# Kernel optimization log

Measured on AMD Instinct MI355X. Metric: run time of the kernel, lower is better.

## Reference

```python
import jax, jax.numpy as jnp
import numpy as np

EPS = 1e-5

def _lin_bn_relu(x, W, b, gamma, beta):
    # x: [N, Cin], W: [Cout, Cin] (torch layout), b/gamma/beta: [Cout]
    y = x @ W.T + b
    mu = jnp.mean(y, axis=0)                      # training-mode batch stats
    var = jnp.mean((y - mu) ** 2, axis=0)         # biased variance (torch BN)
    yhat = (y - mu) * jax.lax.rsqrt(var + EPS)
    return jax.nn.relu(gamma * yhat + beta)


def setup_inputs() -> dict:
    key = jax.random.key(0)
    ks = jax.random.split(key, 16)
    N = 262144
    dims = [(64, 3), (512, 64), (512, 512), (2, 512)]
    inp = {
        "x1": jax.random.normal(ks[0], (8, 4, 8, 8), dtype=jnp.float32),
        "x2": jax.random.normal(ks[1], (N, 3), dtype=jnp.float32),
    }
    for i, (co, ci) in enumerate(dims, start=1):
        lim = 1.0 / np.sqrt(ci)
        inp[f"W{i}"] = jax.random.uniform(ks[2 * i], (co, ci), jnp.float32, -lim, lim)
        inp[f"b{i}"] = jax.random.uniform(ks[2 * i + 1], (co,), jnp.float32, -lim, lim)
    for i, c in enumerate([64, 512, 512], start=1):
        inp[f"gamma{i}"] = jnp.ones((c,), jnp.float32)
        inp[f"beta{i}"] = jnp.zeros((c,), jnp.float32)
    return inp


def reference(x1, x2, W1, b1, W2, b2, W3, b3, W4, b4,
              gamma1, beta1, gamma2, beta2, gamma3, beta3):
    # x1 is sliced in the original forward (x[0][:, 0:-1]) but unused in the output.
    h = _lin_bn_relu(x2, W1, b1, gamma1, beta1)   # [N, 64]
    h = _lin_bn_relu(h, W2, b2, gamma2, beta2)    # [N, 512]
    h = _lin_bn_relu(h, W3, b3, gamma3, beta3)    # [N, 512]
    out = h @ W4.T + b4                           # [N, 2]
    return out
```

## Files before the change

kernel.cpp:

```cpp
#include <hip/hip_runtime.h>

typedef __bf16 bf16x4 __attribute__((ext_vector_type(4)));
typedef __bf16 bf16x8 __attribute__((ext_vector_type(8)));
typedef float f32x4 __attribute__((ext_vector_type(4)));

#define MFMA_BF16 __builtin_amdgcn_mfma_f32_16x16x32_bf16

__global__ __launch_bounds__(256) void prep_xmom_kernel(
    const float* __restrict__ x, const float* __restrict__ W2,
    const float* __restrict__ W3, __bf16* __restrict__ W2bf,
    __bf16* __restrict__ W3bf, float* __restrict__ xmom) {
  const int b = blockIdx.x;
  const int t = threadIdx.x;
  if (b >= 64) {
    const float* src;
    __bf16* dst;
    int idx;
    if (b < 80) {
      idx = (b - 64) * 2048 + t * 8;
      src = W2;
      dst = W2bf;
    } else {
      idx = (b - 80) * 2048 + t * 8;
      src = W3;
      dst = W3bf;
    }
    float4 f0 = *(const float4*)(src + idx);
    float4 f1 = *(const float4*)(src + idx + 4);
    bf16x8 o;
    o[0] = (__bf16)f0.x;
    o[1] = (__bf16)f0.y;
    o[2] = (__bf16)f0.z;
    o[3] = (__bf16)f0.w;
    o[4] = (__bf16)f1.x;
    o[5] = (__bf16)f1.y;
    o[6] = (__bf16)f1.z;
    o[7] = (__bf16)f1.w;
    *(bf16x8*)(dst + idx) = o;
    return;
  }
  float m[9] = {};
#pragma unroll 4
  for (int i = 0; i < 16; ++i) {
    int r = b * 4096 + i * 256 + t;
    const float* xp = x + (size_t)r * 3;
    float a = xp[0], bb = xp[1], c = xp[2];
    m[0] += a;
    m[1] += bb;
    m[2] += c;
    m[3] = fmaf(a, a, m[3]);
    m[4] = fmaf(a, bb, m[4]);
    m[5] = fmaf(a, c, m[5]);
    m[6] = fmaf(bb, bb, m[6]);
    m[7] = fmaf(bb, c, m[7]);
    m[8] = fmaf(c, c, m[8]);
  }
  __shared__ float red[4][9];
  int lane = t & 63, wave = t >> 6;
#pragma unroll
  for (int j = 0; j < 9; ++j) {
    float v = m[j];
    v += __shfl_xor(v, 1);
    v += __shfl_xor(v, 2);
    v += __shfl_xor(v, 4);
    v += __shfl_xor(v, 8);
    v += __shfl_xor(v, 16);
    v += __shfl_xor(v, 32);
    if (lane == 0) red[wave][j] = v;
  }
  __syncthreads();
  if (t < 9) atomicAdd(&xmom[t], red[0][t] + red[1][t] + red[2][t] + red[3][t]);
}

__device__ __forceinline__ void bn1_fold(const float* __restrict__ xm,
                                         const float* __restrict__ W1,
                                         const float* __restrict__ b1,
                                         const float* __restrict__ gamma1,
                                         const float* __restrict__ beta1,
                                         int c, float invN, float fN,
                                         float* f0, float* f1, float* f2,
                                         float* f3) {
  float w0 = W1[c * 3], w1 = W1[c * 3 + 1], w2 = W1[c * 3 + 2], bb = b1[c];
  float wx = w0 * xm[0] + w1 * xm[1] + w2 * xm[2];
  float sy = wx + fN * bb;
  float q = w0 * w0 * xm[3] + 2.f * w0 * w1 * xm[4] + 2.f * w0 * w2 * xm[5] +
            w1 * w1 * xm[6] + 2.f * w1 * w2 * xm[7] + w2 * w2 * xm[8] +
            2.f * bb * wx + fN * bb * bb;
  float mu = sy * invN;
  float var = q * invN - mu * mu;
  float sc = gamma1[c] * rsqrtf(var + 1e-5f);
  float sh = beta1[c] - mu * sc;
  *f0 = sc * w0;
  *f1 = sc * w1;
  *f2 = sc * w2;
  *f3 = sc * bb + sh;
}

__global__ __launch_bounds__(256, 4) void m1_kernel(
    const float* __restrict__ x2, const float* __restrict__ xmom,
    const float* __restrict__ gamma1, const float* __restrict__ beta1,
    const float* __restrict__ W1, const float* __restrict__ b1,
    float* __restrict__ M1, float* __restrict__ s1, float invN, float fN) {
  __shared__ float sF[256];
  __shared__ float xs[768];
  __shared__ __bf16 h1T[64 * 264];
  __shared__ float s1s[4][64];

  const int t = threadIdx.x;
  const int lane = t & 63, wave = t >> 6;
  const int lrow = lane & 15, lgrp = lane >> 4;

  if (t < 64) {
    float f0, f1, f2, f3;
    bn1_fold(xmom, W1, b1, gamma1, beta1, t, invN, fN, &f0, &f1, &f2, &f3);
    sF[t] = f0;
    sF[64 + t] = f1;
    sF[128 + t] = f2;
    sF[192 + t] = f3;
  }
  if (t < 192)
    ((float4*)xs)[t] = ((const float4*)(x2 + (size_t)blockIdx.x * 768))[t];
  __syncthreads();

  const int c0 = (t & 3) * 16;
  const int r0 = t >> 2;
  float sAcc[16] = {};
#pragma unroll
  for (int s = 0; s < 4; ++s) {
    int r = r0 + s * 64;
    float X0 = xs[r * 3], X1 = xs[r * 3 + 1], X2 = xs[r * 3 + 2];
#pragma unroll
    for (int j = 0; j < 16; ++j) {
      int c = c0 + j;
      float h = fmaxf(
          fmaf(sF[c], X0, fmaf(sF[64 + c], X1, fmaf(sF[128 + c], X2, sF[192 + c]))),
          0.f);
      sAcc[j] += h;
      h1T[c * 264 + r] = (__bf16)h;
    }
  }
  __syncthreads();

  f32x4 acc[4] = {};
#pragma unroll
  for (int kk = 0; kk < 256; kk += 32) {
    bf16x8 af = *(const bf16x8*)&h1T[(wave * 16 + lrow) * 264 + kk + lgrp * 8];
#pragma unroll
    for (int n = 0; n < 4; ++n) {
      bf16x8 bfr = *(const bf16x8*)&h1T[(n * 16 + lrow) * 264 + kk + lgrp * 8];
      acc[n] = MFMA_BF16(af, bfr, acc[n], 0, 0, 0);
    }
  }
#pragma unroll
  for (int n = 0; n < 4; ++n)
#pragma unroll
    for (int rr = 0; rr < 4; ++rr)
      atomicAdd(&M1[(wave * 16 + lgrp * 4 + rr) * 64 + n * 16 + lrow],
                acc[n][rr]);

#pragma unroll
  for (int j = 0; j < 16; ++j) {
    float v = sAcc[j];
    v += __shfl_xor(v, 4);
    v += __shfl_xor(v, 8);
    v += __shfl_xor(v, 16);
    v += __shfl_xor(v, 32);
    if (lane < 4) s1s[wave][(lane & 3) * 16 + j] = v;
  }
  __syncthreads();
  if (t < 64)
    atomicAdd(&s1[t], s1s[0][t] + s1s[1][t] + s1s[2][t] + s1s[3][t]);
}

__global__ __launch_bounds__(256) void finalize2v_kernel(
    const float* __restrict__ M1, const float* __restrict__ s1,
    const float* __restrict__ W2, const float* __restrict__ b2,
    const float* __restrict__ gamma2, const float* __restrict__ beta2,
    float* __restrict__ scale2, float* __restrict__ shift2f, float fN) {
  __shared__ float sM[64 * 65];
  __shared__ float ss[64];
  int t = threadIdx.x;
  for (int i = t; i < 4096; i += 256) sM[(i >> 6) * 65 + (i & 63)] = M1[i];
  if (t < 64) ss[t] = s1[t];
  __syncthreads();
  int lane = t & 63;
  int col = blockIdx.x * 4 + (t >> 6);
  float wi = W2[(size_t)col * 64 + lane];
  float p = 0.f;
#pragma unroll
  for (int j = 0; j < 64; ++j) p = fmaf(sM[lane * 65 + j], __shfl(wi, j), p);
  float qi = wi * p;
  float swi = ss[lane] * wi;
#pragma unroll
  for (int off = 1; off < 64; off <<= 1) {
    qi += __shfl_xor(qi, off);
    swi += __shfl_xor(swi, off);
  }
  if (lane == 0) {
    float b = b2[col];
    float sy = swi + fN * b;
    float sqs = qi + 2.f * b * swi + fN * b * b;
    float mu = sy / fN;
    float var = sqs / fN - mu * mu;
    float sc = gamma2[col] * rsqrtf(var + 1e-5f);
    scale2[col] = sc;
    shift2f[col] = (beta2[col] - mu * sc) + sc * b;
  }
}

#define G3_LD(BUF, K)                                                        \
  _Pragma("unroll") for (int m = 0; m < 4; ++m) BUF[m] =                     \
      *(const bf16x8*)&h2r[(m * 16 + lrow) * 520 + (K) * 32 + lgrp * 8];

#define G3_MM(BUF, K)                                                        \
  _Pragma("unroll") for (int m = 0; m < 4; ++m) {                            \
    acc[m][0] = MFMA_BF16(BUF[m], b3r[K][0], acc[m][0], 0, 0, 0);            \
    acc[m][1] = MFMA_BF16(BUF[m], b3r[K][1], acc[m][1], 0, 0, 0);            \
  }

template <int MODE>
__global__ __launch_bounds__(512, 2) void fused_kernel(
    const float* __restrict__ x2, const float* __restrict__ xmom,
    const float* __restrict__ gamma1, const float* __restrict__ beta1,
    const float* __restrict__ W1, const float* __restrict__ b1,
    const __bf16* __restrict__ W2bf, const float* __restrict__ scale2,
    const float* __restrict__ shift2f, const __bf16* __restrict__ W3bf,
    const float* __restrict__ b3, const float* __restrict__ gamma3,
    const float* __restrict__ beta3, const float* __restrict__ W4,
    const float* __restrict__ b4, float* __restrict__ gsum3,
    float* __restrict__ gsq3, float* __restrict__ out,
    __bf16* __restrict__ y3o, int gBase, int gCount, int rStoreRgs,
    float invN, float fN) {
  __shared__ __bf16 h1buf[2][64 * 72];
  __shared__ __bf16 h2buf[2][64 * 520];
  __shared__ float sF[256];
  __shared__ float sSc2[512], sSh2[512];
  __shared__ float outaccW[8][64][2];

  const int t = threadIdx.x;
  const int lane = t & 63, wave = t >> 6;
  const int lrow = lane & 15, lgrp = lane >> 4;
  const int colHalf = blockIdx.x & 1;
  const int rgFirst = gBase + (int)(blockIdx.x >> 1) * gCount;
  const int wCol3 = colHalf * 256 + wave * 32;
  const int wCol2 = wave * 64;

  if (t < 64) {
    float f0, f1, f2, f3;
    bn1_fold(xmom, W1, b1, gamma1, beta1, t, invN, fN, &f0, &f1, &f2, &f3);
    sF[t] = f0;
    sF[64 + t] = f1;
    sF[128 + t] = f2;
    sF[192 + t] = f3;
  }
  sSc2[t] = scale2[t & 511];
  sSh2[t] = shift2f[t & 511];

  bf16x8 b2r[2][4];
#pragma unroll
  for (int kk = 0; kk < 2; ++kk)
#pragma unroll
    for (int n = 0; n < 4; ++n)
      b2r[kk][n] = *(const bf16x8*)&W2bf[(wCol2 + n * 16 + lrow) * 64 +
                                         kk * 32 + lgrp * 8];
  bf16x8 b3r[16][2];
#pragma unroll
  for (int k = 0; k < 16; ++k)
#pragma unroll
    for (int n = 0; n < 2; ++n)
      b3r[k][n] = *(const bf16x8*)&W3bf[(size_t)(wCol3 + n * 16 + lrow) * 512 +
                                        k * 32 + lgrp * 8];

  const int c3a = wCol3 + lrow, c3b = wCol3 + 16 + lrow;
  float b3a = 0.f, b3b = 0.f;
  float sc3a = 0.f, sc3b = 0.f, sh3a = 0.f, sh3b = 0.f;
  float w40a = 0.f, w40b = 0.f, w41a = 0.f, w41b = 0.f, B40 = 0.f, B41 = 0.f;
  if (MODE != 2) {
    b3a = b3[c3a];
    b3b = b3[c3b];
  } else {
    float mu = gsum3[c3a] * invN;
    float var = gsq3[c3a] * invN - mu * mu;
    sc3a = gamma3[c3a] * rsqrtf(var + 1e-5f);
    sh3a = sc3a * b3[c3a] + (beta3[c3a] - mu * sc3a);
    mu = gsum3[c3b] * invN;
    var = gsq3[c3b] * invN - mu * mu;
    sc3b = gamma3[c3b] * rsqrtf(var + 1e-5f);
    sh3b = sc3b * b3[c3b] + (beta3[c3b] - mu * sc3b);
    w40a = W4[c3a];
    w40b = W4[c3b];
    w41a = W4[512 + c3a];
    w41b = W4[512 + c3b];
    B40 = b4[0];
    B41 = b4[1];
  }
  float csA = 0.f, cqA = 0.f, csB = 0.f, cqB = 0.f;

  const int hr = t >> 3, hc0 = (t & 7) * 8;
  const float* xbase = x2 + ((size_t)rgFirst * 64 + hr) * 3;
  float xa, xb, xc;

  auto stageH1 = [&](__bf16* h1p) {
    bf16x8 hv;
#pragma unroll
    for (int j = 0; j < 8; ++j) {
      int c = hc0 + j;
      float h = fmaf(sF[c], xa,
                     fmaf(sF[64 + c], xb, fmaf(sF[128 + c], xc, sF[192 + c])));
      hv[j] = (__bf16)fmaxf(h, 0.f);
    }
    *(bf16x8*)&h1p[hr * 72 + hc0] = hv;
  };

  auto gemm2 = [&](const __bf16* h1p, __bf16* h2p) {
#pragma unroll
    for (int nh = 0; nh < 2; ++nh) {
      f32x4 a2[2][4] = {};
#pragma unroll
      for (int kk = 0; kk < 2; ++kk) {
        bf16x8 af0 = *(const bf16x8*)&h1p[(0 * 16 + lrow) * 72 + kk * 32 + lgrp * 8];
        bf16x8 af1 = *(const bf16x8*)&h1p[(1 * 16 + lrow) * 72 + kk * 32 + lgrp * 8];
        bf16x8 af2 = *(const bf16x8*)&h1p[(2 * 16 + lrow) * 72 + kk * 32 + lgrp * 8];
        bf16x8 af3 = *(const bf16x8*)&h1p[(3 * 16 + lrow) * 72 + kk * 32 + lgrp * 8];
#pragma unroll
        for (int n2 = 0; n2 < 2; ++n2) {
          int n = nh * 2 + n2;
          a2[n2][0] = MFMA_BF16(b2r[kk][n], af0, a2[n2][0], 0, 0, 0);
          a2[n2][1] = MFMA_BF16(b2r[kk][n], af1, a2[n2][1], 0, 0, 0);
          a2[n2][2] = MFMA_BF16(b2r[kk][n], af2, a2[n2][2], 0, 0, 0);
          a2[n2][3] = MFMA_BF16(b2r[kk][n], af3, a2[n2][3], 0, 0, 0);
        }
      }
#pragma unroll
      for (int n2 = 0; n2 < 2; ++n2) {
        int ch0 = wCol2 + (nh * 2 + n2) * 16 + lgrp * 4;
        float s0 = sSc2[ch0], s1v = sSc2[ch0 + 1], s2v = sSc2[ch0 + 2],
              s3v = sSc2[ch0 + 3];
        float z0 = sSh2[ch0], z1 = sSh2[ch0 + 1], z2 = sSh2[ch0 + 2],
              z3 = sSh2[ch0 + 3];
#pragma unroll
        for (int m = 0; m < 4; ++m) {
          int row = m * 16 + lrow;
          bf16x4 hv;
          hv[0] = (__bf16)fmaxf(fmaf(s0, a2[n2][m][0], z0), 0.f);
          hv[1] = (__bf16)fmaxf(fmaf(s1v, a2[n2][m][1], z1), 0.f);
          hv[2] = (__bf16)fmaxf(fmaf(s2v, a2[n2][m][2], z2), 0.f);
          hv[3] = (__bf16)fmaxf(fmaf(s3v, a2[n2][m][3], z3), 0.f);
          *(bf16x4*)&h2p[row * 520 + ch0] = hv;
        }
      }
    }
  };

  __syncthreads();

  xa = xbase[0];
  xb = xbase[1];
  xc = xbase[2];
  stageH1(h1buf[0]);
  __syncthreads();
  gemm2(h1buf[0], h2buf[0]);
  if (gCount > 1) {
    const float* xn = xbase + 192;
    xa = xn[0];
    xb = xn[1];
    xc = xn[2];
    stageH1(h1buf[1]);
  }
  __syncthreads();

  for (int g = 0; g < gCount; ++g) {
    const int rBase = (rgFirst + g) * 64;
    const __bf16* h2r = h2buf[g & 1];
    const bool doStore = (MODE == 3) && (rgFirst + g < rStoreRgs);

    if (g + 2 < gCount) {
      const float* xn = xbase + (size_t)(g + 2) * 192;
      xa = xn[0];
      xb = xn[1];
      xc = xn[2];
    }

    if (g + 1 < gCount) gemm2(h1buf[(g + 1) & 1], h2buf[(g + 1) & 1]);

    if (g + 2 < gCount) stageH1(h1buf[g & 1]);

    f32x4 acc[4][2] = {};
    bf16x8 afA[4], afB[4];
    G3_LD(afA, 0)
#pragma unroll
    for (int k = 0; k < 16; k += 2) {
      G3_LD(afB, k + 1)
      G3_MM(afA, k)
      if (k < 14) { G3_LD(afA, k + 2) }
      G3_MM(afB, k + 1)
    }

    if (MODE != 2) {
#pragma unroll
      for (int m = 0; m < 4; ++m)
#pragma unroll
        for (int rr = 0; rr < 4; ++rr) {
          float ya = acc[m][0][rr] + b3a;
          float yb = acc[m][1][rr] + b3b;
          csA += ya;
          cqA = fmaf(ya, ya, cqA);
          csB += yb;
          cqB = fmaf(yb, yb, cqB);
          if (doStore) {
            size_t row = (size_t)(rBase + m * 16 + lgrp * 4 + rr);
            y3o[row * 512 + c3a] = (__bf16)ya;
            y3o[row * 512 + c3b] = (__bf16)yb;
          }
        }
    } else {
#pragma unroll
      for (int m = 0; m < 4; ++m)
#pragma unroll
        for (int rr = 0; rr < 4; ++rr) {
          float ha = fmaxf(fmaf(sc3a, acc[m][0][rr], sh3a), 0.f);
          float hb = fmaxf(fmaf(sc3b, acc[m][1][rr], sh3b), 0.f);
          float dd0 = fmaf(ha, w40a, hb * w40b);
          float dd1 = fmaf(ha, w41a, hb * w41b);
          dd0 += __shfl_xor(dd0, 1);
          dd1 += __shfl_xor(dd1, 1);
          dd0 += __shfl_xor(dd0, 2);
          dd1 += __shfl_xor(dd1, 2);
          dd0 += __shfl_xor(dd0, 4);
          dd1 += __shfl_xor(dd1, 4);
          dd0 += __shfl_xor(dd0, 8);
          dd1 += __shfl_xor(dd1, 8);
          if (lrow == 0) {
            int row = m * 16 + lgrp * 4 + rr;
            outaccW[wave][row][0] = dd0;
            outaccW[wave][row][1] = dd1;
          }
        }
    }
    __syncthreads();
  }

  if (MODE != 2) {
    csA += __shfl_xor(csA, 16);
    cqA += __shfl_xor(cqA, 16);
    csB += __shfl_xor(csB, 16);
    cqB += __shfl_xor(cqB, 16);
    csA += __shfl_xor(csA, 32);
    cqA += __shfl_xor(cqA, 32);
    csB += __shfl_xor(csB, 32);
    cqB += __shfl_xor(cqB, 32);
    if (lgrp == 0) {
      atomicAdd(&gsum3[c3a], csA);
      atomicAdd(&gsq3[c3a], cqA);
      atomicAdd(&gsum3[c3b], csB);
      atomicAdd(&gsq3[c3b], cqB);
    }
  } else {
    if (t < 128) {
      int row = t >> 1, o = t & 1;
      float s = 0.f;
#pragma unroll
      for (int w = 0; w < 8; ++w) s += outaccW[w][row][o];
      if (colHalf == 0) s += (o == 0) ? B40 : B41;
      atomicAdd(&out[(size_t)(rgFirst * 64 + row) * 2 + o], s);
    }
  }
}

__global__ __launch_bounds__(256) void stream_out_kernel(
    const __bf16* __restrict__ y3, const float* __restrict__ gsum3,
    const float* __restrict__ gsq3, const float* __restrict__ gamma3,
    const float* __restrict__ beta3, const float* __restrict__ W4,
    const float* __restrict__ b4, float* __restrict__ out, int N, float invN) {
  __shared__ float sSc[512], sSh[512], sW0[512], sW1[512];
  int t = threadIdx.x;
  for (int i = t; i < 512; i += 256) {
    float mu = gsum3[i] * invN;
    float var = gsq3[i] * invN - mu * mu;
    float sc = gamma3[i] * rsqrtf(var + 1e-5f);
    sSc[i] = sc;
    sSh[i] = beta3[i] - mu * sc;
    sW0[i] = W4[i];
    sW1[i] = W4[512 + i];
  }
  __syncthreads();
  int lane = t & 63, wv = t >> 6;
  int c0 = lane * 8;
  float fsc[8], fsh[8], fw0[8], fw1[8];
#pragma unroll
  for (int j = 0; j < 8; ++j) {
    fsc[j] = sSc[c0 + j];
    fsh[j] = sSh[c0 + j];
    fw0[j] = sW0[c0 + j];
    fw1[j] = sW1[c0 + j];
  }
  float B0 = b4[0], B1 = b4[1];
  for (size_t row = (size_t)blockIdx.x * 8 + wv * 2; row < (size_t)N;
       row += (size_t)gridDim.x * 8) {
    bf16x8 v0 = *(const bf16x8*)(y3 + row * 512 + c0);
    bf16x8 v1 = *(const bf16x8*)(y3 + (row + 1) * 512 + c0);
    float d0a = 0.f, d1a = 0.f, d0b = 0.f, d1b = 0.f;
#pragma unroll
    for (int j = 0; j < 8; ++j) {
      float ha = fmaxf(fmaf(fsc[j], (float)v0[j], fsh[j]), 0.f);
      float hb = fmaxf(fmaf(fsc[j], (float)v1[j], fsh[j]), 0.f);
      d0a = fmaf(ha, fw0[j], d0a);
      d1a = fmaf(ha, fw1[j], d1a);
      d0b = fmaf(hb, fw0[j], d0b);
      d1b = fmaf(hb, fw1[j], d1b);
    }
    float t0 = d0a + __shfl_xor(d0a, 1);
    float t1 = d1a + __shfl_xor(d1a, 1);
    float t2 = d0b + __shfl_xor(d0b, 1);
    float t3 = d1b + __shfl_xor(d1b, 1);
    float u0 = (lane & 1) ? t1 : t0;
    float u1 = (lane & 1) ? t3 : t2;
    u0 += __shfl_xor(u0, 2);
    u1 += __shfl_xor(u1, 2);
    float w = (lane & 2) ? u1 : u0;
    w += __shfl_xor(w, 4);
    w += __shfl_xor(w, 8);
    w += __shfl_xor(w, 16);
    w += __shfl_xor(w, 32);
    if (lane < 4) out[row * 2 + lane] = w + ((lane & 1) ? B1 : B0);
  }
}

extern "C" void kernel_launch(void* const* d_in, const int* in_sizes, int n_in,
                              void* d_out, int out_size, void* d_ws,
                              size_t ws_size, hipStream_t stream) {
  const float* x2 = (const float*)d_in[1];
  const float* W1 = (const float*)d_in[2];
  const float* b1 = (const float*)d_in[3];
  const float* W2 = (const float*)d_in[4];
  const float* b2 = (const float*)d_in[5];
  const float* W3 = (const float*)d_in[6];
  const float* b3 = (const float*)d_in[7];
  const float* W4 = (const float*)d_in[8];
  const float* b4 = (const float*)d_in[9];
  const float* gamma1 = (const float*)d_in[10];
  const float* beta1 = (const float*)d_in[11];
  const float* gamma2 = (const float*)d_in[12];
  const float* beta2 = (const float*)d_in[13];
  const float* gamma3 = (const float*)d_in[14];
  const float* beta3 = (const float*)d_in[15];
  float* out = (float*)d_out;

  const int N = in_sizes[1] / 3;
  const float invN = 1.0f / (float)N;
  const float fN = (float)N;

  float* f0 = (float*)d_ws;
  float* xmom = f0;
  float* M1 = f0 + 16;
  float* s1 = f0 + 4112;
  float* gsum3 = f0 + 4176;
  float* gsq3 = f0 + 4688;
  float* scale2 = f0 + 5200;
  float* shift2f = f0 + 5712;
  __bf16* W2bf = (__bf16*)(f0 + 6224);
  __bf16* W3bf = W2bf + 32768;

  const size_t y3off = (size_t)1 << 20;
  size_t availRows = (ws_size > y3off) ? (ws_size - y3off) / 1024 : 0;
  int rStoreBlks = (int)((availRows / 1024 < (size_t)(N / 1024))
                             ? availRows / 1024
                             : (size_t)(N / 1024));
  const int rStore = rStoreBlks * 1024;
  __bf16* y3bf = (__bf16*)((char*)d_ws + y3off);

  hipMemsetAsync(f0, 0, 5200 * sizeof(float), stream);
  prep_xmom_kernel<<<208, 256, 0, stream>>>(x2, W2, W3, W2bf, W3bf, xmom);
  m1_kernel<<<N / 256, 256, 0, stream>>>(x2, xmom, gamma1, beta1, W1, b1, M1,
                                         s1, invN, fN);
  finalize2v_kernel<<<128, 256, 0, stream>>>(M1, s1, W2, b2, gamma2, beta2,
                                             scale2, shift2f, fN);

  fused_kernel<3><<<(N / 2048) * 2, 512, 0, stream>>>(
      x2, xmom, gamma1, beta1, W1, b1, W2bf, scale2, shift2f, W3bf, b3,
      gamma3, beta3, W4, b4, gsum3, gsq3, out, y3bf, 0, 32, rStoreBlks * 16,
      invN, fN);

  if (rStore > 0)
    stream_out_kernel<<<2048, 256, 0, stream>>>(y3bf, gsum3, gsq3, gamma3,
                                                beta3, W4, b4, out, rStore,
                                                invN);
  if (rStore < N) {
    hipMemsetAsync(out + (size_t)rStore * 2, 0,
                   (size_t)(N - rStore) * 2 * sizeof(float), stream);
    fused_kernel<2><<<((N - rStore) / 64) * 2, 512, 0, stream>>>(
        x2, xmom, gamma1, beta1, W1, b1, W2bf, scale2, shift2f, W3bf, b3,
        gamma3, beta3, W4, b4, gsum3, gsq3, out, y3bf, rStore / 64, 1, 0,
        invN, fN);
  }
}
```

Before: 324.4 us.

## Merge column-half blocks into 1024-thread blocks covering all 512 layer-3 columns

The fused kernel now launches 1024-thread blocks in which 16 waves each own 32 of the 512 layer-3 columns. Previously two 512-thread blocks each recomputed layer 2 for the same row groups and split the columns between them. This removes the duplicated layer-2 GEMM and the duplicated h1 staging. In the fallback mode it also drops the atomic output accumulation and the memset of the output. In exchange each block holds one resident block per CU (launch_bounds 1024,1), there are fewer row groups per block (16 instead of 32), and block-wide syncs now cover 16 waves.

```diff
diff --git a/kernel.cpp b/kernel.cpp
--- a/kernel.cpp
+++ b/kernel.cpp
@@ -219,7 +219,7 @@
   }
 
 template <int MODE>
-__global__ __launch_bounds__(512, 2) void fused_kernel(
+__global__ __launch_bounds__(1024, 1) void fused_kernel(
     const float* __restrict__ x2, const float* __restrict__ xmom,
     const float* __restrict__ gamma1, const float* __restrict__ beta1,
     const float* __restrict__ W1, const float* __restrict__ b1,
@@ -231,19 +231,18 @@
     float* __restrict__ gsq3, float* __restrict__ out,
     __bf16* __restrict__ y3o, int gBase, int gCount, int rStoreRgs,
     float invN, float fN) {
-  __shared__ __bf16 h1buf[2][64 * 72];
-  __shared__ __bf16 h2buf[2][64 * 520];
+  constexpr int NB = (MODE == 2) ? 1 : 2;
+  __shared__ __bf16 h1buf[NB][64 * 72];
+  __shared__ __bf16 h2buf[NB][64 * 520];
   __shared__ float sF[256];
   __shared__ float sSc2[512], sSh2[512];
-  __shared__ float outaccW[8][64][2];
+  __shared__ float outaccW[(MODE == 2) ? 16 : 1][64][2];
 
   const int t = threadIdx.x;
   const int lane = t & 63, wave = t >> 6;
   const int lrow = lane & 15, lgrp = lane >> 4;
-  const int colHalf = blockIdx.x & 1;
-  const int rgFirst = gBase + (int)(blockIdx.x >> 1) * gCount;
-  const int wCol3 = colHalf * 256 + wave * 32;
-  const int wCol2 = wave * 64;
+  const int rgFirst = gBase + (int)blockIdx.x * gCount;
+  const int wCol = wave * 32;
 
   if (t < 64) {
     float f0, f1, f2, f3;
@@ -253,25 +252,27 @@
     sF[128 + t] = f2;
     sF[192 + t] = f3;
   }
-  sSc2[t] = scale2[t & 511];
-  sSh2[t] = shift2f[t & 511];
-
-  bf16x8 b2r[2][4];
+  if (t < 512) {
+    sSc2[t] = scale2[t];
+    sSh2[t] = shift2f[t];
+  }
+
+  bf16x8 b2r[2][2];
 #pragma unroll
   for (int kk = 0; kk < 2; ++kk)
 #pragma unroll
-    for (int n = 0; n < 4; ++n)
-      b2r[kk][n] = *(const bf16x8*)&W2bf[(wCol2 + n * 16 + lrow) * 64 +
+    for (int n = 0; n < 2; ++n)
+      b2r[kk][n] = *(const bf16x8*)&W2bf[(wCol + n * 16 + lrow) * 64 +
                                          kk * 32 + lgrp * 8];
   bf16x8 b3r[16][2];
 #pragma unroll
   for (int k = 0; k < 16; ++k)
 #pragma unroll
     for (int n = 0; n < 2; ++n)
-      b3r[k][n] = *(const bf16x8*)&W3bf[(size_t)(wCol3 + n * 16 + lrow) * 512 +
+      b3r[k][n] = *(const bf16x8*)&W3bf[(size_t)(wCol + n * 16 + lrow) * 512 +
                                         k * 32 + lgrp * 8];
 
-  const int c3a = wCol3 + lrow, c3b = wCol3 + 16 + lrow;
+  const int c3a = wCol + lrow, c3b = wCol + 16 + lrow;
   float b3a = 0.f, b3b = 0.f;
   float sc3a = 0.f, sc3b = 0.f, sh3a = 0.f, sh3b = 0.f;
   float w40a = 0.f, w40b = 0.f, w41a = 0.f, w41b = 0.f, B40 = 0.f, B41 = 0.f;
@@ -296,58 +297,54 @@
   }
   float csA = 0.f, cqA = 0.f, csB = 0.f, cqB = 0.f;
 
-  const int hr = t >> 3, hc0 = (t & 7) * 8;
+  const int hr = t >> 4, hc0 = (t & 15) * 4;
   const float* xbase = x2 + ((size_t)rgFirst * 64 + hr) * 3;
   float xa, xb, xc;
 
   auto stageH1 = [&](__bf16* h1p) {
-    bf16x8 hv;
-#pragma unroll
-    for (int j = 0; j < 8; ++j) {
+    bf16x4 hv;
+#pragma unroll
+    for (int j = 0; j < 4; ++j) {
       int c = hc0 + j;
       float h = fmaf(sF[c], xa,
                      fmaf(sF[64 + c], xb, fmaf(sF[128 + c], xc, sF[192 + c])));
       hv[j] = (__bf16)fmaxf(h, 0.f);
     }
-    *(bf16x8*)&h1p[hr * 72 + hc0] = hv;
+    *(bf16x4*)&h1p[hr * 72 + hc0] = hv;
   };
 
   auto gemm2 = [&](const __bf16* h1p, __bf16* h2p) {
-#pragma unroll
-    for (int nh = 0; nh < 2; ++nh) {
-      f32x4 a2[2][4] = {};
-#pragma unroll
-      for (int kk = 0; kk < 2; ++kk) {
-        bf16x8 af0 = *(const bf16x8*)&h1p[(0 * 16 + lrow) * 72 + kk * 32 + lgrp * 8];
-        bf16x8 af1 = *(const bf16x8*)&h1p[(1 * 16 + lrow) * 72 + kk * 32 + lgrp * 8];
-        bf16x8 af2 = *(const bf16x8*)&h1p[(2 * 16 + lrow) * 72 + kk * 32 + lgrp * 8];
-        bf16x8 af3 = *(const bf16x8*)&h1p[(3 * 16 + lrow) * 72 + kk * 32 + lgrp * 8];
-#pragma unroll
-        for (int n2 = 0; n2 < 2; ++n2) {
-          int n = nh * 2 + n2;
-          a2[n2][0] = MFMA_BF16(b2r[kk][n], af0, a2[n2][0], 0, 0, 0);
-          a2[n2][1] = MFMA_BF16(b2r[kk][n], af1, a2[n2][1], 0, 0, 0);
-          a2[n2][2] = MFMA_BF16(b2r[kk][n], af2, a2[n2][2], 0, 0, 0);
-          a2[n2][3] = MFMA_BF16(b2r[kk][n], af3, a2[n2][3], 0, 0, 0);
-        }
+    f32x4 a2[2][4] = {};
+#pragma unroll
+    for (int kk = 0; kk < 2; ++kk) {
+      bf16x8 af0 = *(const bf16x8*)&h1p[(0 * 16 + lrow) * 72 + kk * 32 + lgrp * 8];
+      bf16x8 af1 = *(const bf16x8*)&h1p[(1 * 16 + lrow) * 72 + kk * 32 + lgrp * 8];
+      bf16x8 af2 = *(const bf16x8*)&h1p[(2 * 16 + lrow) * 72 + kk * 32 + lgrp * 8];
+      bf16x8 af3 = *(const bf16x8*)&h1p[(3 * 16 + lrow) * 72 + kk * 32 + lgrp * 8];
+#pragma unroll
+      for (int n = 0; n < 2; ++n) {
+        a2[n][0] = MFMA_BF16(b2r[kk][n], af0, a2[n][0], 0, 0, 0);
+        a2[n][1] = MFMA_BF16(b2r[kk][n], af1, a2[n][1], 0, 0, 0);
+        a2[n][2] = MFMA_BF16(b2r[kk][n], af2, a2[n][2], 0, 0, 0);
+        a2[n][3] = MFMA_BF16(b2r[kk][n], af3, a2[n][3], 0, 0, 0);
       }
-#pragma unroll
-      for (int n2 = 0; n2 < 2; ++n2) {
-        int ch0 = wCol2 + (nh * 2 + n2) * 16 + lgrp * 4;
-        float s0 = sSc2[ch0], s1v = sSc2[ch0 + 1], s2v = sSc2[ch0 + 2],
-              s3v = sSc2[ch0 + 3];
-        float z0 = sSh2[ch0], z1 = sSh2[ch0 + 1], z2 = sSh2[ch0 + 2],
-              z3 = sSh2[ch0 + 3];
-#pragma unroll
-        for (int m = 0; m < 4; ++m) {
-          int row = m * 16 + lrow;
-          bf16x4 hv;
-          hv[0] = (__bf16)fmaxf(fmaf(s0, a2[n2][m][0], z0), 0.f);
-          hv[1] = (__bf16)fmaxf(fmaf(s1v, a2[n2][m][1], z1), 0.f);
-          hv[2] = (__bf16)fmaxf(fmaf(s2v, a2[n2][m][2], z2), 0.f);
-          hv[3] = (__bf16)fmaxf(fmaf(s3v, a2[n2][m][3], z3), 0.f);
-          *(bf16x4*)&h2p[row * 520 + ch0] = hv;
-        }
+    }
+#pragma unroll
+    for (int n = 0; n < 2; ++n) {
+      int ch0 = wCol + n * 16 + lgrp * 4;
+      float s0 = sSc2[ch0], s1v = sSc2[ch0 + 1], s2v = sSc2[ch0 + 2],
+            s3v = sSc2[ch0 + 3];
+      float z0 = sSh2[ch0], z1 = sSh2[ch0 + 1], z2 = sSh2[ch0 + 2],
+            z3 = sSh2[ch0 + 3];
+#pragma unroll
+      for (int m = 0; m < 4; ++m) {
+        int row = m * 16 + lrow;
+        bf16x4 hv;
+        hv[0] = (__bf16)fmaxf(fmaf(s0, a2[n][m][0], z0), 0.f);
+        hv[1] = (__bf16)fmaxf(fmaf(s1v, a2[n][m][1], z1), 0.f);
+        hv[2] = (__bf16)fmaxf(fmaf(s2v, a2[n][m][2], z2), 0.f);
+        hv[3] = (__bf16)fmaxf(fmaf(s3v, a2[n][m][3], z3), 0.f);
+        *(bf16x4*)&h2p[row * 520 + ch0] = hv;
       }
     }
   };
@@ -365,13 +362,13 @@
     xa = xn[0];
     xb = xn[1];
     xc = xn[2];
-    stageH1(h1buf[1]);
+    stageH1(h1buf[NB - 1]);
   }
   __syncthreads();
 
   for (int g = 0; g < gCount; ++g) {
     const int rBase = (rgFirst + g) * 64;
-    const __bf16* h2r = h2buf[g & 1];
+    const __bf16* h2r = h2buf[g & (NB - 1)];
     const bool doStore = (MODE == 3) && (rgFirst + g < rStoreRgs);
 
     if (g + 2 < gCount) {
@@ -381,9 +378,10 @@
       xc = xn[2];
     }
 
-    if (g + 1 < gCount) gemm2(h1buf[(g + 1) & 1], h2buf[(g + 1) & 1]);
-
-    if (g + 2 < gCount) stageH1(h1buf[g & 1]);
+    if (g + 1 < gCount)
+      gemm2(h1buf[(g + 1) & (NB - 1)], h2buf[(g + 1) & (NB - 1)]);
+
+    if (g + 2 < gCount) stageH1(h1buf[g & (NB - 1)]);
 
     f32x4 acc[4][2] = {};
     bf16x8 afA[4], afB[4];
@@ -432,8 +430,8 @@
           dd1 += __shfl_xor(dd1, 8);
           if (lrow == 0) {
             int row = m * 16 + lgrp * 4 + rr;
-            outaccW[wave][row][0] = dd0;
-            outaccW[wave][row][1] = dd1;
+            outaccW[(MODE == 2) ? wave : 0][row][0] = dd0;
+            outaccW[(MODE == 2) ? wave : 0][row][1] = dd1;
           }
         }
     }
@@ -460,9 +458,8 @@
       int row = t >> 1, o = t & 1;
       float s = 0.f;
 #pragma unroll
-      for (int w = 0; w < 8; ++w) s += outaccW[w][row][o];
-      if (colHalf == 0) s += (o == 0) ? B40 : B41;
-      atomicAdd(&out[(size_t)(rgFirst * 64 + row) * 2 + o], s);
+      for (int w = 0; w < 16; ++w) s += outaccW[w][row][o];
+      out[(size_t)(rgFirst * 64 + row) * 2 + o] = s + ((o == 0) ? B40 : B41);
     }
   }
 }
@@ -576,9 +573,9 @@
   finalize2v_kernel<<<128, 256, 0, stream>>>(M1, s1, W2, b2, gamma2, beta2,
                                              scale2, shift2f, fN);
 
-  fused_kernel<3><<<(N / 2048) * 2, 512, 0, stream>>>(
+  fused_kernel<3><<<N / 1024, 1024, 0, stream>>>(
       x2, xmom, gamma1, beta1, W1, b1, W2bf, scale2, shift2f, W3bf, b3,
-      gamma3, beta3, W4, b4, gsum3, gsq3, out, y3bf, 0, 32, rStoreBlks * 16,
+      gamma3, beta3, W4, b4, gsum3, gsq3, out, y3bf, 0, 16, rStoreBlks * 16,
       invN, fN);
 
   if (rStore > 0)
@@ -586,9 +583,7 @@
                                                 beta3, W4, b4, out, rStore,
                                                 invN);
   if (rStore < N) {
-    hipMemsetAsync(out + (size_t)rStore * 2, 0,
-                   (size_t)(N - rStore) * 2 * sizeof(float), stream);
-    fused_kernel<2><<<((N - rStore) / 64) * 2, 512, 0, stream>>>(
+    fused_kernel<2><<<(N - rStore) / 64, 1024, 0, stream>>>(
         x2, xmom, gamma1, beta1, W1, b1, W2bf, scale2, shift2f, W3bf, b3,
         gamma3, beta3, W4, b4, gsum3, gsq3, out, y3bf, rStore / 64, 1, 0,
         invN, fN);
```

Result: slower. 520.2 us (+60.4%).
